# Optimization experiments

Hardware: AMD Instinct MI355X
Metric: run time of the kernel (lower is better)

Reference implementation:

```python
import jax, jax.numpy as jnp
import numpy as np


def setup_inputs() -> dict:
    key = jax.random.key(0)
    ks = jax.random.split(key, 5)
    B, H, W, KV = 32, 32, 32, 1024
    N, K, V = 16, 64, 64
    return {
        "key_value": jax.random.normal(ks[0], (B, H, W, KV), dtype=jnp.float32),
        "query": jax.random.normal(ks[1], (1, 1, N, K), dtype=jnp.float32),
        "k_kernel": jax.random.normal(ks[2], (KV, N * K), dtype=jnp.float32) * 0.03,
        "k_bias": jnp.zeros((N * K,), dtype=jnp.float32),
        "v_kernel": jax.random.normal(ks[3], (KV, N * V), dtype=jnp.float32) * 0.03,
        "v_bias": jnp.zeros((N * V,), dtype=jnp.float32),
    }


def reference(key_value, query, k_kernel, k_bias, v_kernel, v_bias):
    # key_value: [B,H,W,KV]; 1x1 conv == channel GEMM
    B, H, W, KV = key_value.shape
    N, K = query.shape[2], query.shape[3]
    V = v_kernel.shape[1] // N
    x = key_value.reshape(B, H * W, KV)                      # [B,HW,KV]
    k = (x @ k_kernel + k_bias).reshape(B, H * W, N, K)       # [B,HW,N,K]
    v = (x @ v_kernel + v_bias).reshape(B, H * W, N, V)       # [B,HW,N,V]
    # single-query dot product per head (no 1/sqrt(K) scaling, per original)
    logits = jnp.einsum('bsnk,nk->bsn', k, query[0, 0])       # [B,HW,N]
    attn = jax.nn.softmax(logits, axis=1)                     # softmax over HW
    out = jnp.einsum('bsn,bsnv->bnv', attn, v)                # [B,N,V]
    return out
```

## Files before the change

### kernel.cpp

```cpp
#include <hip/hip_runtime.h>
#include <hip/hip_fp16.h>


typedef _Float16 f16x8 __attribute__((ext_vector_type(8)));
typedef float f32x4 __attribute__((ext_vector_type(4)));

__device__ __forceinline__ float rlane(float v, int l) {
  return __int_as_float(__builtin_amdgcn_readlane(__float_as_int(v), l));
}

__global__ __launch_bounds__(256) void k_qk(const float* __restrict__ kk,
                                            const float* __restrict__ q,
                                            const float* __restrict__ kb,
                                            __half* __restrict__ qkb,
                                            float* __restrict__ qb) {
  const int gid = blockIdx.x * 256 + threadIdx.x;
  const int c = gid >> 4, n = gid & 15;
  float a = 0.f;
#pragma unroll
  for (int k4 = 0; k4 < 64; k4 += 4) {
    const float4 kv = *(const float4*)(kk + (size_t)c * 1024 + n * 64 + k4);
    const float4 qv = *(const float4*)(q + n * 64 + k4);
    a += kv.x * qv.x + kv.y * qv.y + kv.z * qv.z + kv.w * qv.w;
  }
  const int kbi = c >> 5;
  const int l = (((c >> 3) & 3) << 4) | n;
  const int j = c & 7;
  qkb[kbi * 512 + l * 8 + j] = __float2half(a);
  if (blockIdx.x == 0 && threadIdx.x < 16) {
    float s = 0.f;
    for (int k = 0; k < 64; k++) s += kb[threadIdx.x * 64 + k] * q[threadIdx.x * 64 + k];
    qb[threadIdx.x] = s;
  }
}

__global__ __launch_bounds__(1024, 8) void k_fused(const float* __restrict__ x,
                                                   const __half* __restrict__ qkb,
                                                   const float* __restrict__ qb,
                                                   float* __restrict__ mch,
                                                   float* __restrict__ lch,
                                                   __half* __restrict__ wph) {
  __shared__ __half qkt[16384];
  __shared__ __half ovl[16384];
  __shared__ float et2[64 * 17 + 4];
  __shared__ float etB[64 * 17 + 4];
  const int tid = threadIdx.x;
  const int lane = tid & 63;
  const int wid = tid >> 6;
  const int blk = blockIdx.x;
  const int srow0 = blk * 64;

#pragma unroll
  for (int it = 0; it < 2; ++it) {
    const int g = it * 1024 + tid;
    ((uint4*)qkt)[g] = ((const uint4*)qkb)[g];
  }
  __syncthreads();

  {
    const int wtile = wid & 3;
    const int kq = wid >> 2;
    const int r16 = lane & 15;
    const int khi = lane >> 4;
    const float* xg = x + (size_t)(srow0 + wtile * 16 + r16) * 1024
                        + kq * 256 + khi * 8;
    const __half* qbase = qkt + kq * 4096 + lane * 8;

    f32x4 dacc = {0.f, 0.f, 0.f, 0.f};
    float4 pa0 = *(const float4*)(xg);
    float4 pa1 = *(const float4*)(xg + 4);
    float4 pb0, pb1;

#pragma unroll 1
    for (int kbs = 0; kbs < 8; kbs += 2) {
      pb0 = *(const float4*)(xg + (kbs + 1) * 32);
      pb1 = *(const float4*)(xg + (kbs + 1) * 32 + 4);
      {
        f16x8 af;
        af[0] = (_Float16)pa0.x; af[1] = (_Float16)pa0.y;
        af[2] = (_Float16)pa0.z; af[3] = (_Float16)pa0.w;
        af[4] = (_Float16)pa1.x; af[5] = (_Float16)pa1.y;
        af[6] = (_Float16)pa1.z; af[7] = (_Float16)pa1.w;
        const f16x8 bf = *(const f16x8*)(qbase + kbs * 512);
        dacc = __builtin_amdgcn_mfma_f32_16x16x32_f16(af, bf, dacc, 0, 0, 0);
      }
      if (kbs + 2 < 8) {
        pa0 = *(const float4*)(xg + (kbs + 2) * 32);
        pa1 = *(const float4*)(xg + (kbs + 2) * 32 + 4);
      }
      {
        f16x8 af;
        af[0] = (_Float16)pb0.x; af[1] = (_Float16)pb0.y;
        af[2] = (_Float16)pb0.z; af[3] = (_Float16)pb0.w;
        af[4] = (_Float16)pb1.x; af[5] = (_Float16)pb1.y;
        af[6] = (_Float16)pb1.z; af[7] = (_Float16)pb1.w;
        const f16x8 bf = *(const f16x8*)(qbase + (kbs + 1) * 512);
        dacc = __builtin_amdgcn_mfma_f32_16x16x32_f16(af, bf, dacc, 0, 0, 0);
      }
    }

    const int erow = wtile * 16 + khi * 4;
    if (kq == 0) {
#pragma unroll
      for (int reg = 0; reg < 4; ++reg) et2[(erow + reg) * 17 + r16] = dacc[reg];
    } else if (kq == 2) {
#pragma unroll
      for (int reg = 0; reg < 4; ++reg) etB[(erow + reg) * 17 + r16] = dacc[reg];
    }
    __syncthreads();
    if (kq == 1) {
#pragma unroll
      for (int reg = 0; reg < 4; ++reg) et2[(erow + reg) * 17 + r16] += dacc[reg];
    } else if (kq == 3) {
#pragma unroll
      for (int reg = 0; reg < 4; ++reg) etB[(erow + reg) * 17 + r16] += dacc[reg];
    }
    __syncthreads();
  }

  {
    const int nn = wid;
    const float v = et2[lane * 17 + nn] + etB[lane * 17 + nn] + qb[nn];
    float m = v;
#pragma unroll
    for (int d = 1; d < 64; d <<= 1) m = fmaxf(m, __shfl_xor(m, d));
    const float e = __expf(v - m);
    float s = e;
#pragma unroll
    for (int d = 1; d < 64; d <<= 1) s += __shfl_xor(s, d);
    if (lane == 0) {
      mch[blk * 16 + nn] = m;
      lch[blk * 16 + nn] = s;
    }
    et2[lane * 17 + nn] = e;
  }
  __syncthreads();

  {
    const int sgrp = tid >> 9;
    const int tl = tid & 511;
    const int c0 = tl * 2;
    const int sb = sgrp * 32;
    float acc0[16], acc1[16];
#pragma unroll
    for (int n = 0; n < 16; ++n) { acc0[n] = 0.f; acc1[n] = 0.f; }
    const float* xp = x + (size_t)(srow0 + sb) * 1024 + c0;

    float  ea = et2[(sb + (lane >> 4)) * 17 + (lane & 15)];
    float2 xca[4];
#pragma unroll
    for (int ss = 0; ss < 4; ++ss) xca[ss] = *(const float2*)(xp + (size_t)ss * 1024);

#pragma unroll 1
    for (int sg = 0; sg < 8; ++sg) {
      float  eb = 0.f;
      float2 xcb[4];
      if (sg < 7) {
        const int s0n = (sg + 1) * 4;
        eb = et2[(sb + s0n + (lane >> 4)) * 17 + (lane & 15)];
#pragma unroll
        for (int ss = 0; ss < 4; ++ss)
          xcb[ss] = *(const float2*)(xp + (size_t)(s0n + ss) * 1024);
      }
#pragma unroll
      for (int ss = 0; ss < 4; ++ss) {
#pragma unroll
        for (int n = 0; n < 16; ++n) {
          const float ev = rlane(ea, ss * 16 + n);
          acc0[n] += ev * xca[ss].x;
          acc1[n] += ev * xca[ss].y;
        }
      }
      ea = eb;
#pragma unroll
      for (int ss = 0; ss < 4; ++ss) xca[ss] = xcb[ss];
    }

    if (sgrp == 1) {
#pragma unroll
      for (int n = 0; n < 16; ++n)
        *(__half2*)(ovl + n * 1024 + c0) = __floats2half2_rn(acc0[n], acc1[n]);
    }
    __syncthreads();
    if (sgrp == 0) {
      __half* wpp = wph + (size_t)blk * 16384;
#pragma unroll
      for (int n = 0; n < 16; ++n) {
        const float2 o = __half22float2(*(const __half2*)(ovl + n * 1024 + c0));
        *(__half2*)(wpp + n * 1024 + c0) =
            __floats2half2_rn(acc0[n] + o.x, acc1[n] + o.y);
      }
    }
  }
}

__global__ __launch_bounds__(256) void k_out(const __half* __restrict__ wph,
                                             const float* __restrict__ vk,
                                             const float* __restrict__ vb,
                                             const float* __restrict__ mch,
                                             const float* __restrict__ lch,
                                             float* __restrict__ out) {
  const int bi = blockIdx.x;
  const int b = bi >> 4, n = bi & 15;
  const int tid = threadIdx.x;
  __shared__ float wrow[1024];
  __shared__ float red[4][64];

  float m16[16], l16[16];
#pragma unroll
  for (int ch = 0; ch < 16; ++ch) {
    m16[ch] = mch[(b * 16 + ch) * 16 + n];
    l16[ch] = lch[(b * 16 + ch) * 16 + n];
  }
  float mg = m16[0];
#pragma unroll
  for (int ch = 1; ch < 16; ++ch) mg = fmaxf(mg, m16[ch]);
  float fac[16], lg = 0.f;
#pragma unroll
  for (int ch = 0; ch < 16; ++ch) { fac[ch] = __expf(m16[ch] - mg); lg += fac[ch] * l16[ch]; }

  float4 a4 = {0.f, 0.f, 0.f, 0.f};
#pragma unroll
  for (int ch = 0; ch < 16; ch++) {
    const __half2* p = (const __half2*)(wph + ((size_t)(b * 16 + ch) * 16 + n) * 1024 + tid * 4);
    const float2 f01 = __half22float2(p[0]);
    const float2 f23 = __half22float2(p[1]);
    a4.x += fac[ch] * f01.x; a4.y += fac[ch] * f01.y;
    a4.z += fac[ch] * f23.x; a4.w += fac[ch] * f23.y;
  }
  *(float4*)&wrow[tid * 4] = a4;
  __syncthreads();

  const int v = tid & 63, cq = tid >> 6;
  float a = 0.f;
  const float* vkc = vk + n * 64 + v;
  for (int ci = 0; ci < 256; ci++) {
    const int c = cq * 256 + ci;
    a += wrow[c] * vkc[(size_t)c * 1024];
  }
  red[cq][v] = a;
  __syncthreads();
  if (tid < 64) {
    const float o = (red[0][tid] + red[1][tid] + red[2][tid] + red[3][tid]) / lg
                    + vb[n * 64 + tid];
    out[(size_t)b * 1024 + n * 64 + tid] = o;
  }
}

extern "C" void kernel_launch(void* const* d_in, const int* in_sizes, int n_in,
                              void* d_out, int out_size, void* d_ws, size_t ws_size,
                              hipStream_t stream) {
  const float* x  = (const float*)d_in[0];
  const float* q  = (const float*)d_in[1];
  const float* kk = (const float*)d_in[2];
  const float* kb = (const float*)d_in[3];
  const float* vk = (const float*)d_in[4];
  const float* vb = (const float*)d_in[5];
  float* out = (float*)d_out;

  float*  f   = (float*)d_ws;
  __half* qkb = (__half*)f;
  float*  qb  = f + 8192;
  float*  mch = f + 8208;
  float*  lch = f + 16400;
  __half* wph = (__half*)(f + 24592);

  hipLaunchKernelGGL(k_qk,    dim3(64),  dim3(256),  0, stream, kk, q, kb, qkb, qb);
  hipLaunchKernelGGL(k_fused, dim3(512), dim3(1024), 0, stream, x, qkb, qb, mch, lch, wph);
  hipLaunchKernelGGL(k_out,   dim3(512), dim3(256),  0, stream, wph, vk, vb, mch, lch, out);
}
```

Measured before the change: 68.06 us.

## Compute softmax-weighted x reduction with fp16 MFMA instead of scalar FMAs

Replaces the scalar readlane-broadcast FMA loop that accumulated exp-weights times x over 64 rows with two 16x16x32 f16 MFMA instructions per 16-column tile. Each wave now owns 64 channels and the full 64-row reduction, so the shared-memory overlap buffer and the extra barrier for combining two row groups go away. The aim is to cut VALU work and LDS traffic, at the cost of rounding x and the exp weights to fp16 before accumulation and using strided scalar global loads.

```diff
diff --git a/kernel.cpp b/kernel.cpp
--- a/kernel.cpp
+++ b/kernel.cpp
@@ -4,10 +4,6 @@
 
 typedef _Float16 f16x8 __attribute__((ext_vector_type(8)));
 typedef float f32x4 __attribute__((ext_vector_type(4)));
-
-__device__ __forceinline__ float rlane(float v, int l) {
-  return __int_as_float(__builtin_amdgcn_readlane(__float_as_int(v), l));
-}
 
 __global__ __launch_bounds__(256) void k_qk(const float* __restrict__ kk,
                                             const float* __restrict__ q,
@@ -41,7 +37,6 @@
                                                    float* __restrict__ lch,
                                                    __half* __restrict__ wph) {
   __shared__ __half qkt[16384];
-  __shared__ __half ovl[16384];
   __shared__ float et2[64 * 17 + 4];
   __shared__ float etB[64 * 17 + 4];
   const int tid = threadIdx.x;
@@ -137,59 +132,46 @@
   __syncthreads();
 
   {
-    const int sgrp = tid >> 9;
-    const int tl = tid & 511;
-    const int c0 = tl * 2;
-    const int sb = sgrp * 32;
-    float acc0[16], acc1[16];
-#pragma unroll
-    for (int n = 0; n < 16; ++n) { acc0[n] = 0.f; acc1[n] = 0.f; }
-    const float* xp = x + (size_t)(srow0 + sb) * 1024 + c0;
-
-    float  ea = et2[(sb + (lane >> 4)) * 17 + (lane & 15)];
-    float2 xca[4];
-#pragma unroll
-    for (int ss = 0; ss < 4; ++ss) xca[ss] = *(const float2*)(xp + (size_t)ss * 1024);
-
-#pragma unroll 1
-    for (int sg = 0; sg < 8; ++sg) {
-      float  eb = 0.f;
-      float2 xcb[4];
-      if (sg < 7) {
-        const int s0n = (sg + 1) * 4;
-        eb = et2[(sb + s0n + (lane >> 4)) * 17 + (lane & 15)];
-#pragma unroll
-        for (int ss = 0; ss < 4; ++ss)
-          xcb[ss] = *(const float2*)(xp + (size_t)(s0n + ss) * 1024);
-      }
-#pragma unroll
-      for (int ss = 0; ss < 4; ++ss) {
-#pragma unroll
-        for (int n = 0; n < 16; ++n) {
-          const float ev = rlane(ea, ss * 16 + n);
-          acc0[n] += ev * xca[ss].x;
-          acc1[n] += ev * xca[ss].y;
+    const int r16 = lane & 15;
+    const int sgp = lane >> 4;
+    f16x8 afA, afB;
+#pragma unroll
+    for (int j = 0; j < 8; ++j) {
+      afA[j] = (_Float16)et2[(sgp * 8 + j) * 17 + r16];
+      afB[j] = (_Float16)et2[(32 + sgp * 8 + j) * 17 + r16];
+    }
+    const float* xc = x + (size_t)srow0 * 1024 + wid * 64 + r16;
+    __half* wpp = wph + (size_t)blk * 16384 + wid * 64 + r16;
+
+    float b0a[8], b1a[8], b0b[8], b1b[8];
+#pragma unroll
+    for (int j = 0; j < 8; ++j) {
+      b0a[j] = xc[(size_t)(sgp * 8 + j) * 1024];
+      b1a[j] = xc[(size_t)(32 + sgp * 8 + j) * 1024];
+    }
+#pragma unroll
+    for (int t = 0; t < 4; ++t) {
+      if (t < 3) {
+#pragma unroll
+        for (int j = 0; j < 8; ++j) {
+          b0b[j] = xc[(size_t)(sgp * 8 + j) * 1024 + (t + 1) * 16];
+          b1b[j] = xc[(size_t)(32 + sgp * 8 + j) * 1024 + (t + 1) * 16];
         }
       }
-      ea = eb;
-#pragma unroll
-      for (int ss = 0; ss < 4; ++ss) xca[ss] = xcb[ss];
-    }
-
-    if (sgrp == 1) {
-#pragma unroll
-      for (int n = 0; n < 16; ++n)
-        *(__half2*)(ovl + n * 1024 + c0) = __floats2half2_rn(acc0[n], acc1[n]);
-    }
-    __syncthreads();
-    if (sgrp == 0) {
-      __half* wpp = wph + (size_t)blk * 16384;
-#pragma unroll
-      for (int n = 0; n < 16; ++n) {
-        const float2 o = __half22float2(*(const __half2*)(ovl + n * 1024 + c0));
-        *(__half2*)(wpp + n * 1024 + c0) =
-            __floats2half2_rn(acc0[n] + o.x, acc1[n] + o.y);
-      }
+      f16x8 bf0, bf1;
+#pragma unroll
+      for (int j = 0; j < 8; ++j) {
+        bf0[j] = (_Float16)b0a[j];
+        bf1[j] = (_Float16)b1a[j];
+      }
+      f32x4 dacc = {0.f, 0.f, 0.f, 0.f};
+      dacc = __builtin_amdgcn_mfma_f32_16x16x32_f16(afA, bf0, dacc, 0, 0, 0);
+      dacc = __builtin_amdgcn_mfma_f32_16x16x32_f16(afB, bf1, dacc, 0, 0, 0);
+#pragma unroll
+      for (int reg = 0; reg < 4; ++reg)
+        wpp[(size_t)(sgp * 4 + reg) * 1024 + t * 16] = __float2half(dacc[reg]);
+#pragma unroll
+      for (int j = 0; j < 8; ++j) { b0a[j] = b0b[j]; b1a[j] = b1b[j]; }
     }
   }
 }
```

Result: faster. 65.65 us, median of 3 (-3.5%).
